# Performance work log

Measured on AMD Instinct MI355X. Metric: run time of the kernel, lower is better.

Reference implementation:

```python
import jax, jax.numpy as jnp
import numpy as np

N, D, H = 2048, 1024, 16
HD = D // H  # 64
SCALE = float(np.sqrt(HD))  # sqrt(features // heads) = 8.0


def setup_inputs() -> dict:
    key = jax.random.key(0)
    ks = jax.random.split(key, 9)
    s = 0.02
    return {
        "x": jax.random.normal(ks[0], (N, D), dtype=jnp.float32),
        "Wq": jax.random.normal(ks[1], (D, D), dtype=jnp.float32) * s,
        "bq": jnp.zeros((D,), dtype=jnp.float32),
        "Wk": jax.random.normal(ks[2], (D, D), dtype=jnp.float32) * s,
        "bk": jnp.zeros((D,), dtype=jnp.float32),
        "Wv": jax.random.normal(ks[3], (D, D), dtype=jnp.float32) * s,
        "bv": jnp.zeros((D,), dtype=jnp.float32),
        "Wo": jax.random.normal(ks[4], (D, D), dtype=jnp.float32) * s,
        "bo": jnpp if False else jnp.zeros((D,), dtype=jnp.float32),
    }


def reference(x, Wq, bq, Wk, bk, Wv, bv, Wo, bo):
    # projections: [n, d]
    q = x @ Wq + bq
    k = x @ Wk + bk
    v = x @ Wv + bv
    # split heads: n (h d) -> h n d
    def split(t):
        return t.reshape(N, H, HD).transpose(1, 0, 2)
    q, k, v = split(q), split(k), split(v)
    # attention scores [h, n, n]
    scores = jnp.einsum('hnd,hmd->hnm', q, k) / SCALE
    # causal mask (tril), fill with dtype min as in original
    dmin = jnp.finfo(scores.dtype).min
    mask = jnp.tril(jnp.ones((N, N), dtype=bool))
    scores = jnp.where(mask, scores, dmin)
    attn = jax.nn.softmax(scores, axis=-1)
    # weighted sum, merge heads: h n d -> n (h d)
    out = jnp.einsum('hnm,hmd->hnd', attn, v)
    out = out.transpose(1, 0, 2).reshape(N, D)
    return out @ Wo + bo
```

## Files before the change

kernel.cpp:

```cpp
#include <hip/hip_runtime.h>
#include <hip/hip_bf16.h>
#include <math.h>

#define SA_N 2048
#define SA_D 1024
#define SA_H 16
#define SA_HD 64

typedef __attribute__((ext_vector_type(8))) short bf16x8;
typedef __attribute__((ext_vector_type(4))) float f32x4;
typedef __attribute__((address_space(3))) void lds_t;
typedef __attribute__((address_space(1))) void gmem_t;

#define SC2 0.18033688011112042f

__global__ __launch_bounds__(256) void prep_kernel(
    const float* __restrict__ x,
    const float* __restrict__ Wq, const float* __restrict__ Wk,
    const float* __restrict__ Wv, const float* __restrict__ Wo,
    __hip_bfloat16* __restrict__ xbf, __hip_bfloat16* __restrict__ WtAll)
{
    const int tid = threadIdx.x;
    const int z = blockIdx.z;
    if (z < 2) {
        const int r = z * 1024 + blockIdx.y * 32 + (tid >> 3);
        const int c = blockIdx.x * 32 + (tid & 7) * 4;
        const size_t idx = (size_t)r * SA_D + c;
        float4 v = *reinterpret_cast<const float4*>(&x[idx]);
        union { __hip_bfloat16 hh[4]; short4 s4; } u;
        u.hh[0] = __float2bfloat16(v.x);
        u.hh[1] = __float2bfloat16(v.y);
        u.hh[2] = __float2bfloat16(v.z);
        u.hh[3] = __float2bfloat16(v.w);
        *reinterpret_cast<short4*>(&xbf[idx]) = u.s4;
    } else {
        const int w = z - 2;
        const float* W = (w == 0) ? Wq : (w == 1) ? Wk : (w == 2) ? Wv : Wo;
        const float scale = (w == 0) ? SC2 : 1.0f;
        __hip_bfloat16* Wt = WtAll + (size_t)w * SA_D * SA_D;
        __shared__ float t[32][33];
        const int c0 = blockIdx.x * 32, r0 = blockIdx.y * 32;
        const int tx = tid & 31, ty = tid >> 5;
#pragma unroll
        for (int p = 0; p < 4; ++p)
            t[ty + p * 8][tx] = W[(size_t)(r0 + ty + p * 8) * SA_D + c0 + tx] * scale;
        __syncthreads();
#pragma unroll
        for (int p = 0; p < 4; ++p)
            Wt[(size_t)(c0 + ty + p * 8) * SA_D + r0 + tx] =
                __float2bfloat16(t[tx][ty + p * 8]);
    }
}

__global__ __launch_bounds__(256) void gemm_qkv_kernel(
    const __hip_bfloat16* __restrict__ xbf, const __hip_bfloat16* __restrict__ WtAll,
    const float* __restrict__ bq, const float* __restrict__ bk, const float* __restrict__ bv,
    __hip_bfloat16* __restrict__ Qb, __hip_bfloat16* __restrict__ Kb,
    __hip_bfloat16* __restrict__ VtT)
{
    __shared__ __align__(16) char As[128 * 128];
    __shared__ __align__(16) char Bs[64 * 128];

    const int tid = threadIdx.x;
    const int wave = tid >> 6, lane = tid & 63;
    const int m = lane & 15, quad = lane >> 4;
    const int wm = wave >> 1, wn = wave & 1;
    const int row0 = blockIdx.y * 128;
    const int col0 = blockIdx.x * 64;
    const int w = col0 >> 10;
    const int cw0 = col0 & 1023;
    const __hip_bfloat16* Bt = WtAll + (size_t)w * SA_D * SA_D;

    f32x4 acc[4][2];
#pragma unroll
    for (int mi = 0; mi < 4; ++mi)
#pragma unroll
        for (int ni = 0; ni < 2; ++ni) acc[mi][ni] = (f32x4){0.f, 0.f, 0.f, 0.f};

    const int sr = tid >> 3;
    const int sc = tid & 7;

    for (int k0 = 0; k0 < SA_D; k0 += 64) {
#pragma unroll
        for (int p = 0; p < 4; ++p) {
            const int r = p * 32 + sr;
            const int pc = (sc ^ (r & 7)) * 16;
            const char* ga = (const char*)(xbf + (size_t)(row0 + r) * SA_D + k0) + pc;
            __builtin_amdgcn_global_load_lds((gmem_t*)ga,
                (lds_t*)(As + p * 4096 + wave * 1024), 16, 0, 0);
        }
#pragma unroll
        for (int p = 0; p < 2; ++p) {
            const int r = p * 32 + sr;
            const int pc = (sc ^ (r & 7)) * 16;
            const char* gb = (const char*)(Bt + (size_t)(cw0 + r) * SA_D + k0) + pc;
            __builtin_amdgcn_global_load_lds((gmem_t*)gb,
                (lds_t*)(Bs + p * 4096 + wave * 1024), 16, 0, 0);
        }
        __syncthreads();

#pragma unroll
        for (int s = 0; s < 2; ++s) {
            bf16x8 af[4], bfr[2];
#pragma unroll
            for (int mi = 0; mi < 4; ++mi) {
                const int row = wm * 64 + mi * 16 + m;
                const int pc = (s * 4 + quad) ^ (row & 7);
                af[mi] = *reinterpret_cast<const bf16x8*>(As + row * 128 + pc * 16);
            }
#pragma unroll
            for (int ni = 0; ni < 2; ++ni) {
                const int col = wn * 32 + ni * 16 + m;
                const int pc = (s * 4 + quad) ^ (col & 7);
                bfr[ni] = *reinterpret_cast<const bf16x8*>(Bs + col * 128 + pc * 16);
            }
#pragma unroll
            for (int mi = 0; mi < 4; ++mi)
#pragma unroll
                for (int ni = 0; ni < 2; ++ni)
                    acc[mi][ni] = __builtin_amdgcn_mfma_f32_16x16x32_bf16(
                        af[mi], bfr[ni], acc[mi][ni], 0, 0, 0);
        }
        __syncthreads();
    }

    if (w < 2) {
        __hip_bfloat16* Out = w ? Kb : Qb;
        const float* bb = w ? bk : bq;
        const float bscale = w ? 1.0f : SC2;
#pragma unroll
        for (int ni = 0; ni < 2; ++ni) {
            const int cw = cw0 + wn * 32 + ni * 16 + m;
            const float bvv = bb[cw] * bscale;
#pragma unroll
            for (int mi = 0; mi < 4; ++mi) {
                const int rbase = row0 + wm * 64 + mi * 16 + quad * 4;
#pragma unroll
                for (int reg = 0; reg < 4; ++reg)
                    Out[(size_t)(rbase + reg) * SA_D + cw] =
                        __float2bfloat16(acc[mi][ni][reg] + bvv);
            }
        }
    } else {
#pragma unroll
        for (int ni = 0; ni < 2; ++ni) {
            const int cw = cw0 + wn * 32 + ni * 16 + m;
            const float bvv = bv[cw];
            const int kblk = row0 + wm * 64;
#pragma unroll
            for (int mi = 0; mi < 4; ++mi) {
#pragma unroll
                for (int reg = 0; reg < 4; ++reg) {
                    const int jp = (quad * 4 + reg) * 4 + mi;
                    VtT[(size_t)cw * SA_N + kblk + jp] =
                        __float2bfloat16(acc[mi][ni][reg] + bvv);
                }
            }
        }
    }
}

__global__ __launch_bounds__(256) void gemm_out_kernel(
    const __hip_bfloat16* __restrict__ A, const __hip_bfloat16* __restrict__ Bt,
    const float* __restrict__ bias, float* __restrict__ Cout)
{
    __shared__ __align__(16) char As[64 * 128];
    __shared__ __align__(16) char Bs[64 * 128];
    const int tid = threadIdx.x;
    const int wave = tid >> 6, lane = tid & 63;
    const int m = lane & 15, quad = lane >> 4;
    const int wm = wave >> 1, wn = wave & 1;
    const int row0 = blockIdx.y * 64, col0 = blockIdx.x * 64;

    f32x4 acc[2][2];
#pragma unroll
    for (int i = 0; i < 2; ++i)
#pragma unroll
        for (int j = 0; j < 2; ++j) acc[i][j] = (f32x4){0.f, 0.f, 0.f, 0.f};

    const int sr = tid >> 3;
    const int sc = tid & 7;

    for (int k0 = 0; k0 < SA_D; k0 += 64) {
#pragma unroll
        for (int p = 0; p < 2; ++p) {
            const int r = p * 32 + sr;
            const int pc = (sc ^ (r & 7)) * 16;
            const char* ga = (const char*)(A + (size_t)(row0 + r) * SA_D + k0) + pc;
            __builtin_amdgcn_global_load_lds((gmem_t*)ga,
                (lds_t*)(As + p * 4096 + wave * 1024), 16, 0, 0);
            const char* gb = (const char*)(Bt + (size_t)(col0 + r) * SA_D + k0) + pc;
            __builtin_amdgcn_global_load_lds((gmem_t*)gb,
                (lds_t*)(Bs + p * 4096 + wave * 1024), 16, 0, 0);
        }
        __syncthreads();

#pragma unroll
        for (int s = 0; s < 2; ++s) {
            bf16x8 af[2], bfr[2];
#pragma unroll
            for (int mi = 0; mi < 2; ++mi) {
                const int row = wm * 32 + mi * 16 + m;
                const int pc = (s * 4 + quad) ^ (row & 7);
                af[mi] = *reinterpret_cast<const bf16x8*>(As + row * 128 + pc * 16);
            }
#pragma unroll
            for (int ni = 0; ni < 2; ++ni) {
                const int col = wn * 32 + ni * 16 + m;
                const int pc = (s * 4 + quad) ^ (col & 7);
                bfr[ni] = *reinterpret_cast<const bf16x8*>(Bs + col * 128 + pc * 16);
            }
#pragma unroll
            for (int mi = 0; mi < 2; ++mi)
#pragma unroll
                for (int ni = 0; ni < 2; ++ni)
                    acc[mi][ni] = __builtin_amdgcn_mfma_f32_16x16x32_bf16(
                        af[mi], bfr[ni], acc[mi][ni], 0, 0, 0);
        }
        __syncthreads();
    }

#pragma unroll
    for (int ni = 0; ni < 2; ++ni) {
        const int col = col0 + wn * 32 + ni * 16 + m;
        const float bv = bias[col];
#pragma unroll
        for (int mi = 0; mi < 2; ++mi) {
            const int rbase = row0 + wm * 32 + mi * 16 + quad * 4;
#pragma unroll
            for (int reg = 0; reg < 4; ++reg)
                Cout[(size_t)(rbase + reg) * SA_D + col] = acc[mi][ni][reg] + bv;
        }
    }
}

__global__ __launch_bounds__(512, 4) void flash_mfma_kernel(
    const __hip_bfloat16* __restrict__ Qb,
    const __hip_bfloat16* __restrict__ Kb,
    const __hip_bfloat16* __restrict__ Vt,
    __hip_bfloat16* __restrict__ O)
{
    const int b = blockIdx.x;
    const int h = b & 15;
    const int qraw = b >> 4;
    const int qt = (qraw < 16) ? qraw : 47 - qraw;
    const int row0 = qt * 64;
    const int ntiles = (qt >> 1) + 1;

    const int tid = threadIdx.x;
    const int wave = tid >> 6, lane = tid & 63;
    const int g = wave >> 2, w4 = wave & 3;
    const int ln = lane & 15, quad = lane >> 4;

    __shared__ __align__(16) char Qs[64 * 128];
    __shared__ __align__(16) char Ks[128 * 128];
    __shared__ __align__(16) char Vs[64 * 256];
    __shared__ __align__(16) char Ps[2][64 * 144];
    __shared__ float lmerge[64];

    {
        const int r = wave * 8 + (lane >> 3);
        const int pc = ((lane & 7) ^ (r & 7)) * 16;
        const char* gq = (const char*)(Qb + (size_t)(row0 + r) * SA_D + h * SA_HD) + pc;
        __builtin_amdgcn_global_load_lds((gmem_t*)gq,
            (lds_t*)(Qs + wave * 1024), 16, 0, 0);
    }

    const int kr0 = wave * 8 + (lane >> 3);
    const int kpc = ((lane & 7) ^ (kr0 & 7)) * 16;
    const int vr0 = wave * 4 + (lane >> 4);
    const int vpc = ((lane & 15) ^ (vr0 & 15)) * 16;
    bf16x8 kreg[2], vreg[2];

    auto prefetch = [&](int kt) {
#pragma unroll
        for (int p = 0; p < 2; ++p) {
            kreg[p] = *reinterpret_cast<const bf16x8*>(
                (const char*)(Kb + (size_t)(kt * 128 + p * 64 + kr0) * SA_D + h * SA_HD) + kpc);
            vreg[p] = *reinterpret_cast<const bf16x8*>(
                (const char*)(Vt + (size_t)(h * SA_HD + p * 32 + vr0) * SA_N + kt * 128) + vpc);
        }
    };
    prefetch(0);

    __syncthreads();
    bf16x8 afh[2];
    {
        const int mrow = w4 * 16 + ln;
#pragma unroll
        for (int s = 0; s < 2; ++s) {
            const int pca = (s * 4 + quad) ^ (mrow & 7);
            afh[s] = *reinterpret_cast<const bf16x8*>(Qs + mrow * 128 + pca * 16);
        }
    }

    f32x4 oacc[4], lacc;
#pragma unroll
    for (int dg = 0; dg < 4; ++dg) oacc[dg] = (f32x4){0.f, 0.f, 0.f, 0.f};
    lacc = (f32x4){0.f, 0.f, 0.f, 0.f};

    const short one_bf = (short)0x3F80;
    const bf16x8 ones = {one_bf, one_bf, one_bf, one_bf, one_bf, one_bf, one_bf, one_bf};

    for (int kt = 0; kt < ntiles; ++kt) {
        __syncthreads();
#pragma unroll
        for (int p = 0; p < 2; ++p) {
            *reinterpret_cast<bf16x8*>(Ks + p * 8192 + wave * 1024 + lane * 16) = kreg[p];
            *reinterpret_cast<bf16x8*>(Vs + p * 8192 + wave * 1024 + lane * 16) = vreg[p];
        }
        if (kt + 1 < ntiles) prefetch(kt + 1);
        __syncthreads();

        f32x4 sacc[4];
#pragma unroll
        for (int gg = 0; gg < 4; ++gg) sacc[gg] = (f32x4){0.f, 0.f, 0.f, 0.f};
        __builtin_amdgcn_s_setprio(1);
#pragma unroll
        for (int s = 0; s < 2; ++s) {
#pragma unroll
            for (int gg = 0; gg < 4; ++gg) {
                const int krow = g * 64 + gg * 16 + ln;
                const int pcb = (s * 4 + quad) ^ (krow & 7);
                bf16x8 bf = *reinterpret_cast<const bf16x8*>(Ks + krow * 128 + pcb * 16);
                sacc[gg] = __builtin_amdgcn_mfma_f32_16x16x32_bf16(afh[s], bf, sacc[gg], 0, 0, 0);
            }
        }
        __builtin_amdgcn_s_setprio(0);

        const bool last = (kt == ntiles - 1);
        const int prow_b = w4 * 16 + quad * 4;
        const int qrow_b = row0 + prow_b;
        char* Pg = Ps[g];
#pragma unroll
        for (int reg = 0; reg < 4; ++reg) {
            union { __hip_bfloat16 hh[4]; short4 s4; } u;
#pragma unroll
            for (int gg = 0; gg < 4; ++gg) {
                const int key = kt * 128 + g * 64 + gg * 16 + ln;
                float p = exp2f(sacc[gg][reg]);
                if (last && key > (qrow_b + reg)) p = 0.f;
                u.hh[gg] = __float2bfloat16(p);
            }
            *reinterpret_cast<short4*>(Pg + (prow_b + reg) * 144 + ln * 8) = u.s4;
        }

        __builtin_amdgcn_s_setprio(1);
#pragma unroll
        for (int s2 = 0; s2 < 2; ++s2) {
            bf16x8 pf = *reinterpret_cast<const bf16x8*>(
                Pg + (w4 * 16 + ln) * 144 + s2 * 64 + quad * 16);
            lacc = __builtin_amdgcn_mfma_f32_16x16x32_bf16(pf, ones, lacc, 0, 0, 0);
#pragma unroll
            for (int dg = 0; dg < 4; ++dg) {
                const int vrow = dg * 16 + ln;
                const int kc = g * 8 + s2 * 4 + quad;
                const int pcb = (kc ^ (vrow & 15)) * 16;
                bf16x8 vf = *reinterpret_cast<const bf16x8*>(Vs + vrow * 256 + pcb);
                oacc[dg] = __builtin_amdgcn_mfma_f32_16x16x32_bf16(pf, vf, oacc[dg], 0, 0, 0);
            }
        }
        __builtin_amdgcn_s_setprio(0);
    }

    __syncthreads();
    float* Kf = reinterpret_cast<float*>(Ks);
    if (g == 1) {
#pragma unroll
        for (int reg = 0; reg < 4; ++reg) {
            const int row = w4 * 16 + quad * 4 + reg;
#pragma unroll
            for (int dg = 0; dg < 4; ++dg)
                Kf[row * 64 + dg * 16 + ln] = oacc[dg][reg];
            if (ln == 0) lmerge[row] = lacc[reg];
        }
    }
    __syncthreads();
    if (g == 0) {
#pragma unroll
        for (int reg = 0; reg < 4; ++reg) {
            const int row = w4 * 16 + quad * 4 + reg;
            const float inv = 1.0f / (lacc[reg] + lmerge[row]);
            const int qrow = row0 + row;
#pragma unroll
            for (int dg = 0; dg < 4; ++dg)
                O[(size_t)qrow * SA_D + h * SA_HD + dg * 16 + ln] =
                    __float2bfloat16((oacc[dg][reg] + Kf[row * 64 + dg * 16 + ln]) * inv);
        }
    }
}

extern "C" void kernel_launch(void* const* d_in, const int* in_sizes, int n_in,
                              void* d_out, int out_size, void* d_ws, size_t ws_size,
                              hipStream_t stream) {
    const float* x  = (const float*)d_in[0];
    const float* Wq = (const float*)d_in[1];
    const float* bq = (const float*)d_in[2];
    const float* Wk = (const float*)d_in[3];
    const float* bk = (const float*)d_in[4];
    const float* Wv = (const float*)d_in[5];
    const float* bv = (const float*)d_in[6];
    const float* Wo = (const float*)d_in[7];
    const float* bo = (const float*)d_in[8];
    float* out = (float*)d_out;

    const size_t ND = (size_t)SA_N * SA_D;
    const size_t DD = (size_t)SA_D * SA_D;
    __hip_bfloat16* xbf   = (__hip_bfloat16*)d_ws;
    __hip_bfloat16* WtAll = xbf + ND;
    __hip_bfloat16* Qb    = WtAll + 4 * DD;
    __hip_bfloat16* Kb    = Qb + ND;
    __hip_bfloat16* VtT   = Kb + ND;
    __hip_bfloat16* Abf   = VtT + ND;

    prep_kernel<<<dim3(32, 32, 6), 256, 0, stream>>>(x, Wq, Wk, Wv, Wo, xbf, WtAll);
    gemm_qkv_kernel<<<dim3(3072 / 64, SA_N / 128), 256, 0, stream>>>(
        xbf, WtAll, bq, bk, bv, Qb, Kb, VtT);
    flash_mfma_kernel<<<dim3(512), 512, 0, stream>>>(Qb, Kb, VtT, Abf);
    gemm_out_kernel<<<dim3(SA_D / 64, SA_N / 64), 256, 0, stream>>>(
        Abf, WtAll + 3 * DD, bo, out);
}
```

Baseline: 137.1 us.

## Load K and V MFMA fragments directly from global memory, drop LDS staging

The attention kernel no longer stages K and V tiles through shared memory with register prefetch and two barriers per tile. Each wave now reads its MFMA B-operand fragments straight from global memory (K rows and transposed V). The epilogue merge buffer moves from the K LDS area to the P buffer. This removes the per-tile barriers and LDS traffic and raises occupancy, but loses the software prefetch and relies on cache for the duplicate reads across waves.

```diff
diff --git a/kernel.cpp b/kernel.cpp
--- a/kernel.cpp
+++ b/kernel.cpp
@@ -253,8 +253,6 @@
     const int ln = lane & 15, quad = lane >> 4;
 
     __shared__ __align__(16) char Qs[64 * 128];
-    __shared__ __align__(16) char Ks[128 * 128];
-    __shared__ __align__(16) char Vs[64 * 256];
     __shared__ __align__(16) char Ps[2][64 * 144];
     __shared__ float lmerge[64];
 
@@ -265,25 +263,8 @@
         __builtin_amdgcn_global_load_lds((gmem_t*)gq,
             (lds_t*)(Qs + wave * 1024), 16, 0, 0);
     }
-
-    const int kr0 = wave * 8 + (lane >> 3);
-    const int kpc = ((lane & 7) ^ (kr0 & 7)) * 16;
-    const int vr0 = wave * 4 + (lane >> 4);
-    const int vpc = ((lane & 15) ^ (vr0 & 15)) * 16;
-    bf16x8 kreg[2], vreg[2];
-
-    auto prefetch = [&](int kt) {
-#pragma unroll
-        for (int p = 0; p < 2; ++p) {
-            kreg[p] = *reinterpret_cast<const bf16x8*>(
-                (const char*)(Kb + (size_t)(kt * 128 + p * 64 + kr0) * SA_D + h * SA_HD) + kpc);
-            vreg[p] = *reinterpret_cast<const bf16x8*>(
-                (const char*)(Vt + (size_t)(h * SA_HD + p * 32 + vr0) * SA_N + kt * 128) + vpc);
-        }
-    };
-    prefetch(0);
-
     __syncthreads();
+
     bf16x8 afh[2];
     {
         const int mrow = w4 * 16 + ln;
@@ -302,27 +283,21 @@
     const short one_bf = (short)0x3F80;
     const bf16x8 ones = {one_bf, one_bf, one_bf, one_bf, one_bf, one_bf, one_bf, one_bf};
 
+    const char* Kb8 = (const char*)Kb + (size_t)(g * 64 + ln) * 2048 + h * 128 + quad * 16;
+    const char* Vt8 = (const char*)Vt + (size_t)(h * 64 + ln) * 4096 + (g * 8 + quad) * 16;
+
     for (int kt = 0; kt < ntiles; ++kt) {
-        __syncthreads();
-#pragma unroll
-        for (int p = 0; p < 2; ++p) {
-            *reinterpret_cast<bf16x8*>(Ks + p * 8192 + wave * 1024 + lane * 16) = kreg[p];
-            *reinterpret_cast<bf16x8*>(Vs + p * 8192 + wave * 1024 + lane * 16) = vreg[p];
-        }
-        if (kt + 1 < ntiles) prefetch(kt + 1);
-        __syncthreads();
-
         f32x4 sacc[4];
 #pragma unroll
         for (int gg = 0; gg < 4; ++gg) sacc[gg] = (f32x4){0.f, 0.f, 0.f, 0.f};
+        const char* Kt = Kb8 + (size_t)kt * 128 * 2048;
         __builtin_amdgcn_s_setprio(1);
 #pragma unroll
         for (int s = 0; s < 2; ++s) {
 #pragma unroll
             for (int gg = 0; gg < 4; ++gg) {
-                const int krow = g * 64 + gg * 16 + ln;
-                const int pcb = (s * 4 + quad) ^ (krow & 7);
-                bf16x8 bf = *reinterpret_cast<const bf16x8*>(Ks + krow * 128 + pcb * 16);
+                bf16x8 bf = *reinterpret_cast<const bf16x8*>(
+                    Kt + (size_t)(gg * 16) * 2048 + s * 64);
                 sacc[gg] = __builtin_amdgcn_mfma_f32_16x16x32_bf16(afh[s], bf, sacc[gg], 0, 0, 0);
             }
         }
@@ -345,6 +320,7 @@
             *reinterpret_cast<short4*>(Pg + (prow_b + reg) * 144 + ln * 8) = u.s4;
         }
 
+        const char* Vtk = Vt8 + (size_t)kt * 256;
         __builtin_amdgcn_s_setprio(1);
 #pragma unroll
         for (int s2 = 0; s2 < 2; ++s2) {
@@ -353,10 +329,8 @@
             lacc = __builtin_amdgcn_mfma_f32_16x16x32_bf16(pf, ones, lacc, 0, 0, 0);
 #pragma unroll
             for (int dg = 0; dg < 4; ++dg) {
-                const int vrow = dg * 16 + ln;
-                const int kc = g * 8 + s2 * 4 + quad;
-                const int pcb = (kc ^ (vrow & 15)) * 16;
-                bf16x8 vf = *reinterpret_cast<const bf16x8*>(Vs + vrow * 256 + pcb);
+                bf16x8 vf = *reinterpret_cast<const bf16x8*>(
+                    Vtk + (size_t)(dg * 16) * 4096 + s2 * 64);
                 oacc[dg] = __builtin_amdgcn_mfma_f32_16x16x32_bf16(pf, vf, oacc[dg], 0, 0, 0);
             }
         }
@@ -364,14 +338,14 @@
     }
 
     __syncthreads();
-    float* Kf = reinterpret_cast<float*>(Ks);
+    float* Mf = reinterpret_cast<float*>(Ps);
     if (g == 1) {
 #pragma unroll
         for (int reg = 0; reg < 4; ++reg) {
             const int row = w4 * 16 + quad * 4 + reg;
 #pragma unroll
             for (int dg = 0; dg < 4; ++dg)
-                Kf[row * 64 + dg * 16 + ln] = oacc[dg][reg];
+                Mf[row * 64 + dg * 16 + ln] = oacc[dg][reg];
             if (ln == 0) lmerge[row] = lacc[reg];
         }
     }
@@ -385,7 +359,7 @@
 #pragma unroll
             for (int dg = 0; dg < 4; ++dg)
                 O[(size_t)qrow * SA_D + h * SA_HD + dg * 16 + ln] =
-                    __float2bfloat16((oacc[dg][reg] + Kf[row * 64 + dg * 16 + ln]) * inv);
+                    __float2bfloat16((oacc[dg][reg] + Mf[row * 64 + dg * 16 + ln]) * inv);
         }
     }
 }
```

Measured after the change: 180.2 us. +31.4%, slower.
